# Performance work log

Hardware: AMD Instinct MI355X
Metric: run time of the kernel (lower is better)

## Reference

```python
import jax, jax.numpy as jnp
import numpy as np

N_NODES = 100000
N_EDGES = 1600000
FEAT_DIM = 256
EMBED_DIM = 256


def setup_inputs() -> dict:
    key = jax.random.key(0)
    k1, k2, k3, k4, k5 = jax.random.split(key, 5)
    x = jax.random.normal(k1, (N_NODES, FEAT_DIM), dtype=jnp.float32)
    # Xavier-uniform init for weight [embed_dim, feat_dim]
    limit = float(np.sqrt(6.0 / (EMBED_DIM + FEAT_DIM)))
    weight = jax.random.uniform(k2, (EMBED_DIM, FEAT_DIM), dtype=jnp.float32,
                                minval=-limit, maxval=limit)
    edge_src = jax.random.randint(k3, (N_EDGES,), 0, N_NODES, dtype=jnp.int32)
    edge_dst = jnp.sort(jax.random.randint(k4, (N_EDGES,), 0, N_NODES, dtype=jnp.int32))
    # normalized adjacency values (e.g. D^-1/2 A D^-1/2 entries), positive
    edge_val = jax.random.uniform(k5, (N_EDGES,), dtype=jnp.float32)
    return {"x": x, "weight": weight, "edge_src": edge_src,
            "edge_dst": edge_dst, "edge_val": edge_val}


def reference(x, weight, edge_src, edge_dst, edge_val):
    # Fused GeMM + SpMM: out = A @ (x @ W^T)
    h = jnp.einsum('nf,ef->ne', x, weight)          # [N, embed_dim] dense GEMM
    msgs = h[edge_src] * edge_val[:, None]          # [E, embed_dim] gather + scale
    out = jax.ops.segment_sum(msgs, edge_dst, num_segments=x.shape[0])  # SpMM scatter-add
    return out
```

## Files before the change

kernel.cpp:

```cpp
#include <hip/hip_runtime.h>

#define FEAT 256
#define EMB 256

typedef __attribute__((ext_vector_type(4))) float f32x4;
typedef __attribute__((ext_vector_type(8))) short short8;

__device__ __forceinline__ unsigned cvtpk(float lo, float hi) {
    unsigned r;
    asm volatile("v_cvt_pk_bf16_f32 %0, %1, %2" : "=v"(r) : "v"(lo), "v"(hi));
    return r;
}

__global__ __launch_bounds__(512) void gemm_q8(
    const float* __restrict__ X, const float* __restrict__ W,
    unsigned* __restrict__ H32, float* __restrict__ S, int M) {
    __shared__ ushort As[128][32];
    __shared__ ushort Bs[256][32];

    const int t    = threadIdx.x;
    const int lane = t & 63;
    const int wave = t >> 6;
    const int wr   = (wave >> 2) * 64;
    const int wc   = (wave & 3) * 64;
    const int m0   = blockIdx.x * 128;

    f32x4 acc[4][4] = {};

    const int srow = t >> 3;
    const int sc4  = (t & 7) * 4;
    const int gr0  = m0 + srow;
    const int gr1  = m0 + srow + 64;
    const float* const xp0 = X + (size_t)gr0 * FEAT + sc4;
    const float* const xp1 = X + (size_t)gr1 * FEAT + sc4;
    const float* const wp  = W + (size_t)srow * FEAT + sc4;

    f32x4 xv0 = {0.f, 0.f, 0.f, 0.f}, xv1 = {0.f, 0.f, 0.f, 0.f};
    f32x4 wv[4];
    if (gr0 < M) xv0 = *(const f32x4*)xp0;
    if (gr1 < M) xv1 = *(const f32x4*)xp1;
    #pragma unroll
    for (int j = 0; j < 4; ++j) wv[j] = *(const f32x4*)(wp + (size_t)j * 64 * FEAT);

    for (int k0 = 0; k0 < FEAT; k0 += 32) {
        __syncthreads();
        {
            uint2 u0 = {cvtpk(xv0.x, xv0.y), cvtpk(xv0.z, xv0.w)};
            uint2 u1 = {cvtpk(xv1.x, xv1.y), cvtpk(xv1.z, xv1.w)};
            *(uint2*)&As[srow][sc4]      = u0;
            *(uint2*)&As[srow + 64][sc4] = u1;
            #pragma unroll
            for (int j = 0; j < 4; ++j) {
                uint2 uw = {cvtpk(wv[j].x, wv[j].y), cvtpk(wv[j].z, wv[j].w)};
                *(uint2*)&Bs[srow + 64 * j][sc4] = uw;
            }
        }
        __syncthreads();

        if (k0 + 32 < FEAT) {
            const int kn = k0 + 32;
            xv0 = {0.f, 0.f, 0.f, 0.f};
            xv1 = {0.f, 0.f, 0.f, 0.f};
            if (gr0 < M) xv0 = *(const f32x4*)(xp0 + kn);
            if (gr1 < M) xv1 = *(const f32x4*)(xp1 + kn);
            #pragma unroll
            for (int j = 0; j < 4; ++j)
                wv[j] = *(const f32x4*)(wp + (size_t)j * 64 * FEAT + kn);
        }

        const int r  = lane & 15;
        const int kr = (lane >> 4) * 8;
        short8 a[4], b[4];
        #pragma unroll
        for (int i = 0; i < 4; ++i) a[i] = *(const short8*)&As[wr + i * 16 + r][kr];
        #pragma unroll
        for (int j = 0; j < 4; ++j) b[j] = *(const short8*)&Bs[wc + j * 16 + r][kr];
        #pragma unroll
        for (int i = 0; i < 4; ++i)
            #pragma unroll
            for (int j = 0; j < 4; ++j)
                acc[i][j] = __builtin_amdgcn_mfma_f32_16x16x32_bf16(a[i], b[j], acc[i][j], 0, 0, 0);
    }

    const int g  = lane >> 4;
    const int cc = lane & 15;
    const int b  = wave & 3;
    #pragma unroll
    for (int i = 0; i < 4; ++i) {
        #pragma unroll
        for (int q = 0; q < 4; ++q) {
            const int row = m0 + wr + i * 16 + g * 4 + q;
            float mx = fmaxf(fmaxf(fabsf(acc[i][0][q]), fabsf(acc[i][1][q])),
                             fmaxf(fabsf(acc[i][2][q]), fabsf(acc[i][3][q])));
            mx = fmaxf(mx, __shfl_xor(mx, 1, 64));
            mx = fmaxf(mx, __shfl_xor(mx, 2, 64));
            mx = fmaxf(mx, __shfl_xor(mx, 4, 64));
            mx = fmaxf(mx, __shfl_xor(mx, 8, 64));
            const float inv = mx > 1e-30f ? 127.0f * __builtin_amdgcn_rcpf(mx) : 0.0f;
            if (row < M) {
                unsigned wdw = 0;
                #pragma unroll
                for (int j = 0; j < 4; ++j) {
                    int u = (int)fmaf(acc[i][j][q], inv, 128.5f);
                    u = u < 0 ? 0 : (u > 255 ? 255 : u);
                    wdw |= (unsigned)u << (8 * j);
                }
                H32[(size_t)row * 64 + b * 16 + cc] = wdw;
                if (cc == 0) S[(size_t)row * 4 + b] = mx * (1.0f / 127.0f);
            }
        }
    }
}

__global__ __launch_bounds__(256) void build_rowptr(
    const int* __restrict__ dst, int* __restrict__ rp, int E, int N) {
    int e = blockIdx.x * 256 + threadIdx.x;
    if (e >= E) return;
    int d    = dst[e];
    int prev = (e == 0) ? -1 : dst[e - 1];
    for (int n = prev + 1; n <= d; ++n) rp[n] = e;
    if (e == E - 1) {
        for (int n = d + 1; n <= N; ++n) rp[n] = E;
    }
}

__global__ __launch_bounds__(256) void spmm_q8(
    const uint4* __restrict__ H16, const float* __restrict__ S,
    const int* __restrict__ rp, const int* __restrict__ src,
    const float* __restrict__ val, float* __restrict__ out, int M) {
    const int lane = threadIdx.x & 63;
    const int wave = threadIdx.x >> 6;
    const int li   = lane & 15;
    const int grp  = lane >> 4;
    const int b    = li >> 2;
    const int node = blockIdx.x * 16 + wave * 4 + grp;
    if (node >= M) return;
    const int lo = rp[node], hi = rp[node + 1];

    float a0[16], a1[16];
    #pragma unroll
    for (int k = 0; k < 16; ++k) { a0[k] = 0.f; a1[k] = 0.f; }
    float corr0 = 0.f, corr1 = 0.f;

    for (int e = lo; e < hi; e += 2) {
        const int e1 = e + 1;
        const int c1 = e1 < hi ? e1 : e;
        const int s0 = src[e], s1 = src[c1];
        const float v0 = val[e];
        float v1 = e1 < hi ? val[c1] : 0.f;
        const float vs0 = v0 * S[(size_t)s0 * 4 + b];
        const float vs1 = v1 * S[(size_t)s1 * 4 + b];
        const uint4 p0 = H16[(size_t)s0 * 16 + li];
        const uint4 p1 = H16[(size_t)s1 * 16 + li];
        corr0 += vs0;
        corr1 += vs1;
        const unsigned pd0[4] = {p0.x, p0.y, p0.z, p0.w};
        const unsigned pd1[4] = {p1.x, p1.y, p1.z, p1.w};
        #pragma unroll
        for (int d = 0; d < 4; ++d) {
            #pragma unroll
            for (int j = 0; j < 4; ++j) {
                a0[d * 4 + j] += vs0 * (float)((pd0[d] >> (8 * j)) & 0xffu);
                a1[d * 4 + j] += vs1 * (float)((pd1[d] >> (8 * j)) & 0xffu);
            }
        }
    }

    const float corr = (corr0 + corr1) * 128.0f;
    float* const obase = out + (size_t)node * EMB + b * 64 + (li & 3) * 4;
    #pragma unroll
    for (int j = 0; j < 4; ++j) {
        f32x4 o = {a0[j]      + a1[j]      - corr,
                   a0[4 + j]  + a1[4 + j]  - corr,
                   a0[8 + j]  + a1[8 + j]  - corr,
                   a0[12 + j] + a1[12 + j] - corr};
        __builtin_nontemporal_store(o, (f32x4*)(obase + j * 16));
    }
}

extern "C" void kernel_launch(void* const* d_in, const int* in_sizes, int n_in,
                              void* d_out, int out_size, void* d_ws, size_t ws_size,
                              hipStream_t stream) {
    const float* x    = (const float*)d_in[0];
    const float* w    = (const float*)d_in[1];
    const int*   esrc = (const int*)d_in[2];
    const int*   edst = (const int*)d_in[3];
    const float* eval = (const float*)d_in[4];

    const int M = in_sizes[0] / FEAT;
    const int E = in_sizes[2];

    unsigned* Hbuf = (unsigned*)d_ws;
    float*    S    = (float*)((char*)d_ws + (size_t)M * 256);
    int*      rp   = (int*)((char*)S + (size_t)M * 4 * sizeof(float));

    gemm_q8<<<(M + 127) / 128, 512, 0, stream>>>(x, w, Hbuf, S, M);
    build_rowptr<<<(E + 255) / 256, 256, 0, stream>>>(edst, rp, E, M);
    spmm_q8<<<(M + 15) / 16, 256, 0, stream>>>((const uint4*)Hbuf, S, rp, esrc, eval,
                                               (float*)d_out, M);
}
```

Baseline: 127.2 us.

## Double-buffer LDS tiles in GEMM to halve barriers per K step

Shared-memory A and B tiles are now double-buffered. The next tile is converted and stored into the alternate buffer after the MFMAs on the current one, and global prefetch runs two steps ahead. This drops one __syncthreads per K iteration and lets LDS writes overlap other waves' compute. In exchange LDS use doubles, which may reduce occupancy, and the GEMM is only one part of a pipeline likely dominated by the SpMM.

```diff
diff --git a/kernel.cpp b/kernel.cpp
--- a/kernel.cpp
+++ b/kernel.cpp
@@ -15,8 +15,8 @@
 __global__ __launch_bounds__(512) void gemm_q8(
     const float* __restrict__ X, const float* __restrict__ W,
     unsigned* __restrict__ H32, float* __restrict__ S, int M) {
-    __shared__ ushort As[128][32];
-    __shared__ ushort Bs[256][32];
+    __shared__ ushort As[2][128][32];
+    __shared__ ushort Bs[2][256][32];
 
     const int t    = threadIdx.x;
     const int lane = t & 63;
@@ -35,51 +35,71 @@
     const float* const xp1 = X + (size_t)gr1 * FEAT + sc4;
     const float* const wp  = W + (size_t)srow * FEAT + sc4;
 
+    const int r  = lane & 15;
+    const int kr = (lane >> 4) * 8;
+
     f32x4 xv0 = {0.f, 0.f, 0.f, 0.f}, xv1 = {0.f, 0.f, 0.f, 0.f};
     f32x4 wv[4];
     if (gr0 < M) xv0 = *(const f32x4*)xp0;
     if (gr1 < M) xv1 = *(const f32x4*)xp1;
     #pragma unroll
     for (int j = 0; j < 4; ++j) wv[j] = *(const f32x4*)(wp + (size_t)j * 64 * FEAT);
-
+    {
+        uint2 u0 = {cvtpk(xv0.x, xv0.y), cvtpk(xv0.z, xv0.w)};
+        uint2 u1 = {cvtpk(xv1.x, xv1.y), cvtpk(xv1.z, xv1.w)};
+        *(uint2*)&As[0][srow][sc4]      = u0;
+        *(uint2*)&As[0][srow + 64][sc4] = u1;
+        #pragma unroll
+        for (int j = 0; j < 4; ++j) {
+            uint2 uw = {cvtpk(wv[j].x, wv[j].y), cvtpk(wv[j].z, wv[j].w)};
+            *(uint2*)&Bs[0][srow + 64 * j][sc4] = uw;
+        }
+    }
+    xv0 = {0.f, 0.f, 0.f, 0.f};
+    xv1 = {0.f, 0.f, 0.f, 0.f};
+    if (gr0 < M) xv0 = *(const f32x4*)(xp0 + 32);
+    if (gr1 < M) xv1 = *(const f32x4*)(xp1 + 32);
+    #pragma unroll
+    for (int j = 0; j < 4; ++j) wv[j] = *(const f32x4*)(wp + (size_t)j * 64 * FEAT + 32);
+    __syncthreads();
+
+    int cur = 0;
     for (int k0 = 0; k0 < FEAT; k0 += 32) {
-        __syncthreads();
-        {
-            uint2 u0 = {cvtpk(xv0.x, xv0.y), cvtpk(xv0.z, xv0.w)};
-            uint2 u1 = {cvtpk(xv1.x, xv1.y), cvtpk(xv1.z, xv1.w)};
-            *(uint2*)&As[srow][sc4]      = u0;
-            *(uint2*)&As[srow + 64][sc4] = u1;
-            #pragma unroll
-            for (int j = 0; j < 4; ++j) {
-                uint2 uw = {cvtpk(wv[j].x, wv[j].y), cvtpk(wv[j].z, wv[j].w)};
-                *(uint2*)&Bs[srow + 64 * j][sc4] = uw;
-            }
-        }
-        __syncthreads();
-
-        if (k0 + 32 < FEAT) {
-            const int kn = k0 + 32;
-            xv0 = {0.f, 0.f, 0.f, 0.f};
-            xv1 = {0.f, 0.f, 0.f, 0.f};
-            if (gr0 < M) xv0 = *(const f32x4*)(xp0 + kn);
-            if (gr1 < M) xv1 = *(const f32x4*)(xp1 + kn);
-            #pragma unroll
-            for (int j = 0; j < 4; ++j)
-                wv[j] = *(const f32x4*)(wp + (size_t)j * 64 * FEAT + kn);
-        }
-
-        const int r  = lane & 15;
-        const int kr = (lane >> 4) * 8;
         short8 a[4], b[4];
         #pragma unroll
-        for (int i = 0; i < 4; ++i) a[i] = *(const short8*)&As[wr + i * 16 + r][kr];
-        #pragma unroll
-        for (int j = 0; j < 4; ++j) b[j] = *(const short8*)&Bs[wc + j * 16 + r][kr];
+        for (int i = 0; i < 4; ++i) a[i] = *(const short8*)&As[cur][wr + i * 16 + r][kr];
+        #pragma unroll
+        for (int j = 0; j < 4; ++j) b[j] = *(const short8*)&Bs[cur][wc + j * 16 + r][kr];
         #pragma unroll
         for (int i = 0; i < 4; ++i)
             #pragma unroll
             for (int j = 0; j < 4; ++j)
                 acc[i][j] = __builtin_amdgcn_mfma_f32_16x16x32_bf16(a[i], b[j], acc[i][j], 0, 0, 0);
+
+        if (k0 + 32 < FEAT) {
+            const int nxt = cur ^ 1;
+            uint2 u0 = {cvtpk(xv0.x, xv0.y), cvtpk(xv0.z, xv0.w)};
+            uint2 u1 = {cvtpk(xv1.x, xv1.y), cvtpk(xv1.z, xv1.w)};
+            *(uint2*)&As[nxt][srow][sc4]      = u0;
+            *(uint2*)&As[nxt][srow + 64][sc4] = u1;
+            #pragma unroll
+            for (int j = 0; j < 4; ++j) {
+                uint2 uw = {cvtpk(wv[j].x, wv[j].y), cvtpk(wv[j].z, wv[j].w)};
+                *(uint2*)&Bs[nxt][srow + 64 * j][sc4] = uw;
+            }
+            if (k0 + 64 < FEAT) {
+                const int kn = k0 + 64;
+                xv0 = {0.f, 0.f, 0.f, 0.f};
+                xv1 = {0.f, 0.f, 0.f, 0.f};
+                if (gr0 < M) xv0 = *(const f32x4*)(xp0 + kn);
+                if (gr1 < M) xv1 = *(const f32x4*)(xp1 + kn);
+                #pragma unroll
+                for (int j = 0; j < 4; ++j)
+                    wv[j] = *(const f32x4*)(wp + (size_t)j * 64 * FEAT + kn);
+            }
+            __syncthreads();
+            cur ^= 1;
+        }
     }
 
     const int g  = lane >> 4;
```

New measurement: 135.1 us. +6.2%, slower.

## Reorder quantized H layout so SpMM slices columns across blocks

Applied to the files above, without the earlier changes.

The GEMM epilogue now transposes the packed int8 bytes through shared memory so each 32-bit word holds four contiguous output columns, and stores the per-row scales block-major. The SpMM is split into 8 column slices per node group, each thread handling 4 columns with one 32-bit gather per edge instead of a 16-byte gather, and edge index/value loads become nontemporal. This cuts registers per thread and raises parallelism, with the aim of making adjacent column slices of the same rows hit L2 together. The cost is that the edge lists and row pointers are read 8 times, and the epilogue gains an extra LDS round trip.

```diff
diff --git a/kernel.cpp b/kernel.cpp
--- a/kernel.cpp
+++ b/kernel.cpp
@@ -17,6 +17,7 @@
     unsigned* __restrict__ H32, float* __restrict__ S, int M) {
     __shared__ ushort As[128][32];
     __shared__ ushort Bs[256][32];
+    __shared__ unsigned lbuf[512];
 
     const int t    = threadIdx.x;
     const int lane = t & 63;
@@ -85,6 +86,8 @@
     const int g  = lane >> 4;
     const int cc = lane & 15;
     const int b  = wave & 3;
+    const int sel  = cc >> 2;
+    const int rbase = wave * 64 + g * 16 + 4 * (cc & 3);
     #pragma unroll
     for (int i = 0; i < 4; ++i) {
         #pragma unroll
@@ -97,16 +100,22 @@
             mx = fmaxf(mx, __shfl_xor(mx, 4, 64));
             mx = fmaxf(mx, __shfl_xor(mx, 8, 64));
             const float inv = mx > 1e-30f ? 127.0f * __builtin_amdgcn_rcpf(mx) : 0.0f;
+            unsigned wdw = 0;
+            #pragma unroll
+            for (int j = 0; j < 4; ++j) {
+                int u = (int)fmaf(acc[i][j][q], inv, 128.5f);
+                u = u < 0 ? 0 : (u > 255 ? 255 : u);
+                wdw |= (unsigned)u << (8 * j);
+            }
+            lbuf[t] = wdw;
+            uint4 d = *(const uint4*)&lbuf[rbase];
+            unsigned o = ((d.x >> (8 * sel)) & 0xffu)
+                       | (((d.y >> (8 * sel)) & 0xffu) << 8)
+                       | (((d.z >> (8 * sel)) & 0xffu) << 16)
+                       | (((d.w >> (8 * sel)) & 0xffu) << 24);
             if (row < M) {
-                unsigned wdw = 0;
-                #pragma unroll
-                for (int j = 0; j < 4; ++j) {
-                    int u = (int)fmaf(acc[i][j][q], inv, 128.5f);
-                    u = u < 0 ? 0 : (u > 255 ? 255 : u);
-                    wdw |= (unsigned)u << (8 * j);
-                }
-                H32[(size_t)row * 64 + b * 16 + cc] = wdw;
-                if (cc == 0) S[(size_t)row * 4 + b] = mx * (1.0f / 127.0f);
+                H32[(size_t)row * 64 + b * 16 + cc] = o;
+                if (cc == 0) S[(size_t)b * M + row] = mx * (1.0f / 127.0f);
             }
         }
     }
@@ -125,57 +134,46 @@
 }
 
 __global__ __launch_bounds__(256) void spmm_q8(
-    const uint4* __restrict__ H16, const float* __restrict__ S,
+    const unsigned* __restrict__ H32, const float* __restrict__ S,
     const int* __restrict__ rp, const int* __restrict__ src,
     const float* __restrict__ val, float* __restrict__ out, int M) {
-    const int lane = threadIdx.x & 63;
-    const int wave = threadIdx.x >> 6;
-    const int li   = lane & 15;
-    const int grp  = lane >> 4;
-    const int b    = li >> 2;
-    const int node = blockIdx.x * 16 + wave * 4 + grp;
+    const int t     = threadIdx.x;
+    const int li    = t & 7;
+    const int grp   = t >> 3;
+    const int slice = blockIdx.x & 7;
+    const int node  = (blockIdx.x >> 3) * 32 + grp;
     if (node >= M) return;
+    const float* const Sb = S + (size_t)(slice >> 1) * M;
+    const int doff = slice * 8 + li;
     const int lo = rp[node], hi = rp[node + 1];
 
-    float a0[16], a1[16];
-    #pragma unroll
-    for (int k = 0; k < 16; ++k) { a0[k] = 0.f; a1[k] = 0.f; }
-    float corr0 = 0.f, corr1 = 0.f;
+    float a0[4] = {0.f, 0.f, 0.f, 0.f}, a1[4] = {0.f, 0.f, 0.f, 0.f};
+    float c0 = 0.f, c1 = 0.f;
 
     for (int e = lo; e < hi; e += 2) {
         const int e1 = e + 1;
-        const int c1 = e1 < hi ? e1 : e;
-        const int s0 = src[e], s1 = src[c1];
-        const float v0 = val[e];
-        float v1 = e1 < hi ? val[c1] : 0.f;
-        const float vs0 = v0 * S[(size_t)s0 * 4 + b];
-        const float vs1 = v1 * S[(size_t)s1 * 4 + b];
-        const uint4 p0 = H16[(size_t)s0 * 16 + li];
-        const uint4 p1 = H16[(size_t)s1 * 16 + li];
-        corr0 += vs0;
-        corr1 += vs1;
-        const unsigned pd0[4] = {p0.x, p0.y, p0.z, p0.w};
-        const unsigned pd1[4] = {p1.x, p1.y, p1.z, p1.w};
+        const int k1 = e1 < hi ? e1 : e;
+        const int s0 = __builtin_nontemporal_load(src + e);
+        const int s1 = __builtin_nontemporal_load(src + k1);
+        const float v0 = __builtin_nontemporal_load(val + e);
+        const float v1 = e1 < hi ? __builtin_nontemporal_load(val + k1) : 0.f;
+        const float vs0 = v0 * Sb[s0];
+        const float vs1 = v1 * Sb[s1];
+        const unsigned p0 = H32[(size_t)s0 * 64 + doff];
+        const unsigned p1 = H32[(size_t)s1 * 64 + doff];
+        c0 += vs0;
+        c1 += vs1;
         #pragma unroll
-        for (int d = 0; d < 4; ++d) {
-            #pragma unroll
-            for (int j = 0; j < 4; ++j) {
-                a0[d * 4 + j] += vs0 * (float)((pd0[d] >> (8 * j)) & 0xffu);
-                a1[d * 4 + j] += vs1 * (float)((pd1[d] >> (8 * j)) & 0xffu);
-            }
+        for (int j = 0; j < 4; ++j) {
+            a0[j] += vs0 * (float)((p0 >> (8 * j)) & 0xffu);
+            a1[j] += vs1 * (float)((p1 >> (8 * j)) & 0xffu);
         }
     }
 
-    const float corr = (corr0 + corr1) * 128.0f;
-    float* const obase = out + (size_t)node * EMB + b * 64 + (li & 3) * 4;
-    #pragma unroll
-    for (int j = 0; j < 4; ++j) {
-        f32x4 o = {a0[j]      + a1[j]      - corr,
-                   a0[4 + j]  + a1[4 + j]  - corr,
-                   a0[8 + j]  + a1[8 + j]  - corr,
-                   a0[12 + j] + a1[12 + j] - corr};
-        __builtin_nontemporal_store(o, (f32x4*)(obase + j * 16));
-    }
+    const float corr = (c0 + c1) * 128.0f;
+    f32x4 o = {a0[0] + a1[0] - corr, a0[1] + a1[1] - corr,
+               a0[2] + a1[2] - corr, a0[3] + a1[3] - corr};
+    __builtin_nontemporal_store(o, (f32x4*)(out + (size_t)node * EMB + doff * 4));
 }
 
 extern "C" void kernel_launch(void* const* d_in, const int* in_sizes, int n_in,
@@ -196,6 +194,6 @@
 
     gemm_q8<<<(M + 127) / 128, 512, 0, stream>>>(x, w, Hbuf, S, M);
     build_rowptr<<<(E + 255) / 256, 256, 0, stream>>>(edst, rp, E, M);
-    spmm_q8<<<(M + 15) / 16, 256, 0, stream>>>((const uint4*)Hbuf, S, rp, esrc, eval,
-                                               (float*)d_out, M);
+    const int nb = (M + 31) / 32;
+    spmm_q8<<<nb * 8, 256, 0, stream>>>(Hbuf, S, rp, esrc, eval, (float*)d_out, M);
 }
```

New measurement: 482.7 us. 280% more time.
